# Performance work log

Measured on AMD Instinct MI355X. Metric: run time of the kernel, lower is better.

## Reference

```python
import jax, jax.numpy as jnp
import numpy as np

# ---- geometry constants (LinearProbeGeom) ----
N_DET, N_T = 128, 2048
NX, NY = 128, 256
PITCH, DT = 3.0e-4, 2.5e-8
C_SOUND = 1540.0
X0, DX = 0.0, 3.0e-4
Y0, DY = 1.0e-3, 1.5e-4
ARRAY_X0, ARRAY_Y = 0.0, 0.0

_freq = np.fft.rfftfreq(N_T, d=DT).astype(np.float32)
OMEGA = jnp.asarray(2.0 * np.pi * _freq, dtype=jnp.float32)            # [n_f]
KX = jnp.asarray((2.0 * np.pi * np.fft.fftfreq(N_DET, d=PITCH)).astype(np.float32))  # [n_det]
_fw = np.ones(_freq.shape[0], dtype=np.float32)
if _fw.shape[0] > 2:
    _fw[1:-1] = 2.0
if N_T % 2 == 0 and _fw.shape[0] > 1:
    _fw[-1] = 1.0
FREQ_W = jnp.asarray(_fw)                                              # [n_f]
XC = jnp.asarray((X0 + np.arange(NX) * DX - ARRAY_X0).astype(np.float32))  # [nx]
YC = jnp.asarray((Y0 + np.arange(NY) * DY - ARRAY_Y).astype(np.float32))   # [ny]


def setup_inputs() -> dict:
    key = jax.random.key(0)
    sino = jax.random.normal(key, (8, 2, N_DET, N_T), dtype=jnp.float32)
    # Hann window apodization (non-trainable buffer in the torch module)
    win = 0.5 - 0.5 * np.cos(2 * np.pi * np.arange(N_DET) / max(N_DET - 1, 1))
    apod = jnp.asarray(win.astype(np.float32))
    return {"sino": sino, "apod": apod}


def reference(sino, apod):
    B, C, n_det, n_t = sino.shape
    eps = jnp.finfo(jnp.float32).eps
    # per-(B,C) standardization over (n_det, n_t)
    mean = sino.mean(axis=(-2, -1), keepdims=True)
    sn = sino - mean
    std = jnp.sqrt(jnp.mean(sn * sn, axis=(-2, -1), keepdims=True) + eps)
    sn = sn / std
    sw = sn * apod[None, None, :, None]
    # temporal rFFT then spatial FFT over detectors -> [B,C,n_det,n_f] complex64
    spec = jnp.fft.fft(jnp.fft.rfft(sw, axis=-1), axis=2)
    kz_sq = (OMEGA / C_SOUND)[None, :] ** 2 - (KX ** 2)[:, None]       # [n_det,n_f]
    kz = jnp.sqrt(jnp.clip(kz_sq, 0.0))
    spec = spec * (kz_sq > 0).astype(spec.dtype)
    # phase factors (vectorized over all ny depths -> one big contraction)
    phase_x = jnp.exp(1j * KX[:, None] * XC[None, :]).astype(spec.dtype)        # [n_det,nx]
    phase_y = jnp.exp(1j * YC[:, None, None] * kz[None, :, :]).astype(spec.dtype)  # [ny,n_det,n_f]
    specw = spec * FREQ_W.astype(spec.dtype)[None, None, None, :]
    band = jnp.einsum('bcdf,ydf->bcyd', specw, phase_y)                # sum over freq
    img_c = jnp.einsum('bcyd,dx->bcyx', band, phase_x)                 # [B,C,ny,nx]
    img = jnp.abs(img_c).astype(sino.dtype)
    norm = jnp.maximum(apod.sum(), eps) * jnp.maximum(FREQ_W.sum(), eps)
    return img / norm
```

## Files before the change

### kernel.cpp

```cpp
#include <hip/hip_runtime.h>
#include <math.h>

#define N_DETC 128
#define N_TC   2048
#define N_FC   1025
#define N_FP   1056
#define NXC    128
#define NYC    256
#define NBCC   16

#define MPAD(i) ((i) + ((i) >> 5))

typedef short bf16x8 __attribute__((ext_vector_type(8)));
typedef float f32x4  __attribute__((ext_vector_type(4)));

__device__ __forceinline__ float2 cmulf(float2 a, float2 b){
    return make_float2(a.x*b.x - a.y*b.y, a.x*b.y + a.y*b.x);
}

#if __has_builtin(__builtin_amdgcn_sinf) && __has_builtin(__builtin_amdgcn_cosf)
__device__ __forceinline__ float sin_rev(float tf){ return __builtin_amdgcn_sinf(tf); }
__device__ __forceinline__ float cos_rev(float tf){ return __builtin_amdgcn_cosf(tf); }
#else
__device__ __forceinline__ float sin_rev(float tf){ return __sinf(6.28318530718f * tf); }
__device__ __forceinline__ float cos_rev(float tf){ return __cosf(6.28318530718f * tf); }
#endif

__device__ __forceinline__ ushort cvt_bf16(float x){
    uint u = __float_as_uint(x);
    return (ushort)((u + 0x7FFFu + ((u >> 16) & 1u)) >> 16);
}

__global__ __launch_bounds__(256) void k_stats1(const float* __restrict__ sino,
                                                float* __restrict__ psum,
                                                float* __restrict__ psq){
    int bc    = blockIdx.x >> 6;
    int chunk = blockIdx.x & 63;
    const float4* p = (const float4*)(sino + (size_t)bc * (N_DETC * N_TC)) + (size_t)chunk * 1024;
    float s = 0.f, q = 0.f;
    #pragma unroll
    for (int i = 0; i < 4; ++i){
        float4 v = p[threadIdx.x + i * 256];
        s += v.x + v.y + v.z + v.w;
        q += v.x*v.x + v.y*v.y + v.z*v.z + v.w*v.w;
    }
    #pragma unroll
    for (int m = 1; m < 64; m <<= 1){
        s += __shfl_xor(s, m, 64);
        q += __shfl_xor(q, m, 64);
    }
    __shared__ float ls[4], lq[4];
    int w = threadIdx.x >> 6, lane = threadIdx.x & 63;
    if (lane == 0){ ls[w] = s; lq[w] = q; }
    __syncthreads();
    if (threadIdx.x == 0){
        psum[blockIdx.x] = ls[0] + ls[1] + ls[2] + ls[3];
        psq[blockIdx.x]  = lq[0] + lq[1] + lq[2] + lq[3];
    }
}

__global__ __launch_bounds__(256) void k_tfft(const float* __restrict__ sino,
                                              const float* __restrict__ apod,
                                              const float* __restrict__ psum,
                                              const float* __restrict__ psq,
                                              float2* __restrict__ spec){
    int row = blockIdx.x;
    int bc = row >> 7, d = row & 127;
    __shared__ float2 z[1055];
    __shared__ float sm[2];
    int tid = threadIdx.x;
    if (tid < 64){
        float s = psum[bc * 64 + tid], q = psq[bc * 64 + tid];
        #pragma unroll
        for (int m = 1; m < 64; m <<= 1){
            s += __shfl_xor(s, m, 64);
            q += __shfl_xor(q, m, 64);
        }
        if (tid == 0){
            const float inv_n = 1.f / (float)(N_DETC * N_TC);
            float mean = s * inv_n;
            float var  = q * inv_n - mean * mean;
            sm[0] = mean;
            sm[1] = rsqrtf(fmaxf(var, 0.f) + 1.1920929e-7f);
        }
    }
    __syncthreads();
    float mean = sm[0];
    float scl  = sm[1] * apod[d];
    const float2* p = (const float2*)(sino + (size_t)row * N_TC);
    for (int n = tid; n < 1024; n += 256){
        float2 v = p[n];
        int r = __brev((unsigned)n) >> 22;
        z[MPAD(r)] = make_float2((v.x - mean) * scl, (v.y - mean) * scl);
    }
    __syncthreads();
    #pragma unroll
    for (int st = 0; st < 5; ++st){
        int h = 1 << (2 * st);
        int q = tid;
        int k = q & (h - 1);
        int g = q >> (2 * st);
        int base = (g << (2 * st + 2)) + k;
        float2 x0 = z[MPAD(base)];
        float2 x1 = z[MPAD(base + h)];
        float2 x2 = z[MPAD(base + 2 * h)];
        float2 x3 = z[MPAD(base + 3 * h)];
        float a1 = -(float)M_PI * (float)k / (float)h;
        float s1, c1; __sincosf(a1, &s1, &c1);
        float a2 = 0.5f * a1;
        float s2, c2; __sincosf(a2, &s2, &c2);
        float2 t1 = make_float2(x1.x * c1 - x1.y * s1, x1.x * s1 + x1.y * c1);
        float2 t3 = make_float2(x3.x * c1 - x3.y * s1, x3.x * s1 + x3.y * c1);
        float2 y0 = make_float2(x0.x + t1.x, x0.y + t1.y);
        float2 y1 = make_float2(x0.x - t1.x, x0.y - t1.y);
        float2 y2 = make_float2(x2.x + t3.x, x2.y + t3.y);
        float2 y3 = make_float2(x2.x - t3.x, x2.y - t3.y);
        float2 u = make_float2(y2.x * c2 - y2.y * s2, y2.x * s2 + y2.y * c2);
        float2 v = make_float2(y3.x * c2 - y3.y * s2, y3.x * s2 + y3.y * c2);
        float2 w = make_float2(v.y, -v.x);
        z[MPAD(base)]         = make_float2(y0.x + u.x, y0.y + u.y);
        z[MPAD(base + 2 * h)] = make_float2(y0.x - u.x, y0.y - u.y);
        z[MPAD(base + h)]     = make_float2(y1.x + w.x, y1.y + w.y);
        z[MPAD(base + 3 * h)] = make_float2(y1.x - w.x, y1.y - w.y);
        __syncthreads();
    }
    float2* o = spec + (size_t)row * N_FC;
    for (int k = tid; k < 1025; k += 256){
        float2 A  = z[MPAD(k & 1023)];
        float2 Bv = z[MPAD((1024 - k) & 1023)];
        float Br = Bv.x, Bi = -Bv.y;
        float Er = 0.5f * (A.x + Br), Ei = 0.5f * (A.y + Bi);
        float Dr = 0.5f * (A.x - Br), Di = 0.5f * (A.y - Bi);
        float Or = Di, Oi = -Dr;
        float ang = -(float)M_PI * (float)k * (1.0f / 1024.0f);
        float sn, cs; __sincosf(ang, &sn, &cs);
        float Xr = Er + cs * Or - sn * Oi;
        float Xi = Ei + cs * Oi + sn * Or;
        o[k] = make_float2(Xr, Xi);
    }
}

__global__ __launch_bounds__(256) void k_dft(const float2* __restrict__ spec,
                                             ushort* __restrict__ Arp,
                                             ushort* __restrict__ Aip,
                                             float4* __restrict__ kzJ){
    int bid = blockIdx.x;
    int ft = bid >> 4, bc = bid & 15;
    int f0 = ft << 5;
    int tid = threadIdx.x;
    __shared__ float2 tile[128][33];
    __shared__ ushort stAr[128][40];
    __shared__ ushort stAi[128][40];

    int fl  = tid & 31;
    int kd0 = tid >> 5;
    int f = f0 + fl;
    bool fok = (f <= 1024);
    float fr = (float)f * 19531.25f;
    float oc = fr * (1.0f / 1540.0f);

    #pragma unroll
    for (int i = 0; i < 16; ++i){
        int kd = kd0 + (i << 3);
        int rkd = __brev((unsigned)kd) >> 25;
        float2 v = fok ? spec[((size_t)(bc * 128 + kd)) * N_FC + f] : make_float2(0.f, 0.f);
        tile[rkd][fl] = v;
    }
    if (bc == 0){
        #pragma unroll
        for (int i = 0; i < 16; ++i){
            int kd = kd0 + (i << 3);
            int sdx = (kd < 64) ? kd : kd - 128;
            float bb = (float)sdx * 26.0416666f;
            float kq = oc * oc - bb * bb;
            float kzr = (fok && kq > 0.f) ? sqrtf(kq) : 0.f;
            float tj = 1.5e-4f * kzr;
            tj -= floorf(tj);
            kzJ[(size_t)kd * N_FP + f] = make_float4(kzr, cos_rev(tj), sin_rev(tj), 0.f);
        }
    }
    __syncthreads();
    #pragma unroll
    for (int st = 0; st < 3; ++st){
        int h = 1 << (2 * st);
        #pragma unroll
        for (int it = 0; it < 4; ++it){
            int task = tid + (it << 8);
            int ff = task & 31;
            int q  = task >> 5;
            int k = q & (h - 1);
            int g = q >> (2 * st);
            int base = (g << (2 * st + 2)) + k;
            float2 x0 = tile[base][ff];
            float2 x1 = tile[base + h][ff];
            float2 x2 = tile[base + 2 * h][ff];
            float2 x3 = tile[base + 3 * h][ff];
            float a1 = -(float)M_PI * (float)k / (float)h;
            float s1, c1; __sincosf(a1, &s1, &c1);
            float a2 = 0.5f * a1;
            float s2, c2; __sincosf(a2, &s2, &c2);
            float2 t1 = make_float2(x1.x * c1 - x1.y * s1, x1.x * s1 + x1.y * c1);
            float2 t3 = make_float2(x3.x * c1 - x3.y * s1, x3.x * s1 + x3.y * c1);
            float2 y0 = make_float2(x0.x + t1.x, x0.y + t1.y);
            float2 y1 = make_float2(x0.x - t1.x, x0.y - t1.y);
            float2 y2 = make_float2(x2.x + t3.x, x2.y + t3.y);
            float2 y3 = make_float2(x2.x - t3.x, x2.y - t3.y);
            float2 u = make_float2(y2.x * c2 - y2.y * s2, y2.x * s2 + y2.y * c2);
            float2 v = make_float2(y3.x * c2 - y3.y * s2, y3.x * s2 + y3.y * c2);
            float2 w = make_float2(v.y, -v.x);
            tile[base][ff]         = make_float2(y0.x + u.x, y0.y + u.y);
            tile[base + 2 * h][ff] = make_float2(y0.x - u.x, y0.y - u.y);
            tile[base + h][ff]     = make_float2(y1.x + w.x, y1.y + w.y);
            tile[base + 3 * h][ff] = make_float2(y1.x - w.x, y1.y - w.y);
        }
        __syncthreads();
    }
    #pragma unroll
    for (int it = 0; it < 8; ++it){
        int task = tid + (it << 8);
        int ff = task & 31, j = task >> 5;
        int i1 = j, i2 = j + 64;
        float ang = -(float)M_PI * (float)j * (1.0f / 64.0f);
        float sn, cs; __sincosf(ang, &sn, &cs);
        float2 u = tile[i1][ff], v = tile[i2][ff];
        float2 t = make_float2(v.x * cs - v.y * sn, v.x * sn + v.y * cs);
        tile[i1][ff] = make_float2(u.x + t.x, u.y + t.y);
        tile[i2][ff] = make_float2(u.x - t.x, u.y - t.y);
    }
    __syncthreads();
    float fw = (f == 0 || f == 1024) ? 1.f : 2.f;
    #pragma unroll
    for (int i = 0; i < 16; ++i){
        int kd = kd0 + (i << 3);
        int sdx = (kd < 64) ? kd : kd - 128;
        float bb = (float)sdx * 26.0416666f;
        float m = (fok && (oc * oc - bb * bb > 0.f)) ? fw : 0.f;
        float2 v = tile[kd][fl];
        stAr[kd][fl] = cvt_bf16(v.x * m);
        stAi[kd][fl] = cvt_bf16(v.y * m);
    }
    __syncthreads();
    int kds = tid >> 1, hf = tid & 1;
    size_t rowoff = ((size_t)kds * 16 + bc) * N_FP + f0 + hf * 16;
    uint4 r0 = *(const uint4*)&stAr[kds][hf * 16];
    uint4 r1 = *(const uint4*)&stAr[kds][hf * 16 + 8];
    uint4 i0 = *(const uint4*)&stAi[kds][hf * 16];
    uint4 i1v = *(const uint4*)&stAi[kds][hf * 16 + 8];
    ((uint4*)(Arp + rowoff))[0] = r0;
    ((uint4*)(Arp + rowoff))[1] = r1;
    ((uint4*)(Aip + rowoff))[0] = i0;
    ((uint4*)(Aip + rowoff))[1] = i1v;
}

__global__ __launch_bounds__(512) void k_band(const ushort* __restrict__ Ar,
                                              const ushort* __restrict__ Ai,
                                              const float4* __restrict__ kzJ,
                                              float2* __restrict__ band_p){
    int blk = blockIdx.x;
    int fc = blk & 1;
    int yh = (blk >> 1) & 1;
    int kd = blk >> 2;
    int nt = fc ? 17 : 16;
    int tid  = threadIdx.x;
    int wid  = tid >> 6;
    int lane = tid & 63;
    int fp = tid & 15;
    int yq = tid >> 4;
    float ymg = 1.0e-3f + 1.5e-4f * (float)(yh * 128 + yq * 4);

    __shared__ ushort Bls[2][2][128][40];

    int arow = lane & 15;
    int koff = (lane >> 4) * 8;
    int ylocal = wid * 16 + arow;
    const ushort* Arp = Ar + ((size_t)kd * 16 + arow) * N_FP + koff + fc * 512;
    const ushort* Aip = Ai + ((size_t)kd * 16 + arow) * N_FP + koff + fc * 512;
    const float4* kjb = kzJ + (size_t)kd * N_FP + fc * 512;

    auto GENC = [&](float4 k0, float4 k1, int buf){
        float t0 = ymg * k0.x; t0 -= floorf(t0);
        float t1 = ymg * k1.x; t1 -= floorf(t1);
        float cA = cos_rev(t0), sA = sin_rev(t0);
        float cB = cos_rev(t1), sB = sin_rev(t1);
        #pragma unroll
        for (int j = 0; j < 4; ++j){
            int y = yq * 4 + j;
            uint br, bi;
            asm("v_cvt_pk_bf16_f32 %0, %1, %2" : "=v"(br) : "v"(cA), "v"(cB));
            asm("v_cvt_pk_bf16_f32 %0, %1, %2" : "=v"(bi) : "v"(sA), "v"(sB));
            *(uint*)&Bls[buf][0][y][fp * 2] = br;
            *(uint*)&Bls[buf][1][y][fp * 2] = bi;
            if (j < 3){
                float nA = fmaf(cA, k0.y, -(sA * k0.z));
                float mA = fmaf(sA, k0.y,  (cA * k0.z));
                cA = nA; sA = mA;
                float nB = fmaf(cB, k1.y, -(sB * k1.z));
                float mB = fmaf(sB, k1.y,  (cB * k1.z));
                cB = nB; sB = mB;
            }
        }
    };

    f32x4 P1 = {0.f,0.f,0.f,0.f}, P2 = P1, P3 = P1, P4 = P1;

    bf16x8 car = *(const bf16x8*)(Arp);
    bf16x8 cai = *(const bf16x8*)(Aip);
    GENC(kjb[fp * 2], kjb[fp * 2 + 1], 0);
    __syncthreads();

    for (int t = 0; t < nt; ++t){
        bf16x8 nar, nai;
        float4 k0, k1;
        if (t < nt - 1){
            nar = *(const bf16x8*)(Arp + (t + 1) * 32);
            nai = *(const bf16x8*)(Aip + (t + 1) * 32);
            k0 = kjb[(t + 1) * 32 + fp * 2];
            k1 = kjb[(t + 1) * 32 + fp * 2 + 1];
        }
        int buf = t & 1;
        bf16x8 br = *(const bf16x8*)&Bls[buf][0][ylocal][koff];
        bf16x8 bi = *(const bf16x8*)&Bls[buf][1][ylocal][koff];
        P1 = __builtin_amdgcn_mfma_f32_16x16x32_bf16(car, br, P1, 0, 0, 0);
        P2 = __builtin_amdgcn_mfma_f32_16x16x32_bf16(cai, bi, P2, 0, 0, 0);
        P3 = __builtin_amdgcn_mfma_f32_16x16x32_bf16(car, bi, P3, 0, 0, 0);
        P4 = __builtin_amdgcn_mfma_f32_16x16x32_bf16(cai, br, P4, 0, 0, 0);
        if (t < nt - 1){
            GENC(k0, k1, buf ^ 1);
        }
        __syncthreads();
        if (t < nt - 1){ car = nar; cai = nai; }
    }

    int y = yh * 128 + wid * 16 + (lane & 15);
    #pragma unroll
    for (int r = 0; r < 4; ++r){
        int bc = (lane >> 4) * 4 + r;
        band_p[(((size_t)fc * 128 + kd) * 16 + bc) * 256 + y] = make_float2(P1[r] - P2[r], P3[r] + P4[r]);
    }
}

__global__ __launch_bounds__(256) void k_final(const float2* __restrict__ band_p,
                                               const float* __restrict__ apod,
                                               float* __restrict__ out){
    int blk = blockIdx.x;
    int bc = blk >> 5, yt = blk & 31;
    __shared__ float2 tile[128][9];
    __shared__ float asum;
    int tid = threadIdx.x;
    if (tid < 64){
        float a = apod[tid] + apod[tid + 64];
        #pragma unroll
        for (int m = 1; m < 64; m <<= 1) a += __shfl_xor(a, m, 64);
        if (tid == 0) asum = a;
    }
    #pragma unroll
    for (int k2 = 0; k2 < 4; ++k2){
        int idx = tid + k2 * 256;
        int kd = idx >> 3, yi = idx & 7;
        size_t o0 = (((size_t)0 * 128 + kd) * 16 + bc) * 256 + yt * 8 + yi;
        size_t o1 = (((size_t)1 * 128 + kd) * 16 + bc) * 256 + yt * 8 + yi;
        float2 a = band_p[o0], b = band_p[o1];
        int rkd = __brev((unsigned)kd) >> 25;
        tile[rkd][yi] = make_float2(a.x + b.x, a.y + b.y);
    }
    __syncthreads();
    #pragma unroll
    for (int st = 0; st < 3; ++st){
        int h = 1 << (2 * st);
        int q  = tid >> 3;
        int yi = tid & 7;
        int k = q & (h - 1);
        int g = q >> (2 * st);
        int base = (g << (2 * st + 2)) + k;
        float2 x0 = tile[base][yi];
        float2 x1 = tile[base + h][yi];
        float2 x2 = tile[base + 2 * h][yi];
        float2 x3 = tile[base + 3 * h][yi];
        float a1 = (float)M_PI * (float)k / (float)h;
        float s1, c1; __sincosf(a1, &s1, &c1);
        float a2 = 0.5f * a1;
        float s2, c2; __sincosf(a2, &s2, &c2);
        float2 t1 = make_float2(x1.x * c1 - x1.y * s1, x1.x * s1 + x1.y * c1);
        float2 t3 = make_float2(x3.x * c1 - x3.y * s1, x3.x * s1 + x3.y * c1);
        float2 y0 = make_float2(x0.x + t1.x, x0.y + t1.y);
        float2 y1 = make_float2(x0.x - t1.x, x0.y - t1.y);
        float2 y2 = make_float2(x2.x + t3.x, x2.y + t3.y);
        float2 y3 = make_float2(x2.x - t3.x, x2.y - t3.y);
        float2 u = make_float2(y2.x * c2 - y2.y * s2, y2.x * s2 + y2.y * c2);
        float2 v = make_float2(y3.x * c2 - y3.y * s2, y3.x * s2 + y3.y * c2);
        float2 w = make_float2(-v.y, v.x);
        tile[base][yi]         = make_float2(y0.x + u.x, y0.y + u.y);
        tile[base + 2 * h][yi] = make_float2(y0.x - u.x, y0.y - u.y);
        tile[base + h][yi]     = make_float2(y1.x + w.x, y1.y + w.y);
        tile[base + 3 * h][yi] = make_float2(y1.x - w.x, y1.y - w.y);
        __syncthreads();
    }
    #pragma unroll
    for (int it = 0; it < 2; ++it){
        int task = tid + (it << 8);
        int yi = task & 7, j = task >> 3;
        float ang = (float)M_PI * (float)j * (1.0f / 64.0f);
        float sn, cs; __sincosf(ang, &sn, &cs);
        float2 u = tile[j][yi], v = tile[j + 64][yi];
        float2 t = make_float2(v.x * cs - v.y * sn, v.x * sn + v.y * cs);
        tile[j][yi]      = make_float2(u.x + t.x, u.y + t.y);
        tile[j + 64][yi] = make_float2(u.x - t.x, u.y - t.y);
    }
    __syncthreads();
    float invnorm = 1.f / (fmaxf(asum, 1.1920929e-7f) * 2048.f);
    #pragma unroll
    for (int k2 = 0; k2 < 4; ++k2){
        int idx = tid + k2 * 256;
        int x = idx & 127, yi = idx >> 7;
        float2 v = tile[x][yi];
        int y = yt * 8 + yi;
        out[((size_t)bc * 256 + y) * 128 + x] = sqrtf(v.x * v.x + v.y * v.y) * invnorm;
    }
}

extern "C" void kernel_launch(void* const* d_in, const int* in_sizes, int n_in,
                              void* d_out, int out_size, void* d_ws, size_t ws_size,
                              hipStream_t stream){
    const float* sino = (const float*)d_in[0];
    const float* apod = (const float*)d_in[1];
    float* out = (float*)d_out;
    float* W = (float*)d_ws;
    float* psum = W + 64;
    float* psq  = W + 1088;
    float2* spec  = (float2*)(W + 2112);
    ushort* Arp   = (ushort*)(W + 2112 + 4198400);
    ushort* Aip   = Arp + (size_t)16 * 128 * N_FP;
    float4* kzJ   = (float4*)(W + 2112 + 4198400 + 2162688);
    float2* band_p = spec;

    k_stats1<<<NBCC * 64, 256, 0, stream>>>(sino, psum, psq);
    k_tfft  <<<NBCC * N_DETC, 256, 0, stream>>>(sino, apod, psum, psq, spec);
    k_dft   <<<33 * 16, 256, 0, stream>>>(spec, Arp, Aip, kzJ);
    k_band  <<<512, 512, 0, stream>>>(Arp, Aip, kzJ, band_p);
    k_final <<<NBCC * 32, 256, 0, stream>>>(band_p, apod, out);
}
```

Before: 69.83 us.

## Fuse stats into temporal FFT, defer normalization, store spectrum as bf16

Removes the separate statistics kernel. Each temporal-FFT block now accumulates per-row sum and sum-of-squares while running the FFT on raw data. Mean subtraction (only the DC bin changes) and the apodization/std scaling move into the spatial DFT kernel, which works because the FFT is linear. The intermediate spectrum is packed to bf16 pairs, halving its write and read traffic, at the cost of reduced precision before normalization.

```diff
diff --git a/kernel.cpp b/kernel.cpp
--- a/kernel.cpp
+++ b/kernel.cpp
@@ -31,75 +31,41 @@
     return (ushort)((u + 0x7FFFu + ((u >> 16) & 1u)) >> 16);
 }
 
-__global__ __launch_bounds__(256) void k_stats1(const float* __restrict__ sino,
-                                                float* __restrict__ psum,
-                                                float* __restrict__ psq){
-    int bc    = blockIdx.x >> 6;
-    int chunk = blockIdx.x & 63;
-    const float4* p = (const float4*)(sino + (size_t)bc * (N_DETC * N_TC)) + (size_t)chunk * 1024;
+__global__ __launch_bounds__(256) void k_tfft(const float* __restrict__ sino,
+                                              float* __restrict__ psum,
+                                              float* __restrict__ psq,
+                                              uint* __restrict__ spec_u){
+    int row = blockIdx.x;
+    __shared__ float2 z[1055];
+    __shared__ float ls[4], lq[4];
+    int tid = threadIdx.x;
+    const float2* p = (const float2*)(sino + (size_t)row * N_TC);
     float s = 0.f, q = 0.f;
-    #pragma unroll
-    for (int i = 0; i < 4; ++i){
-        float4 v = p[threadIdx.x + i * 256];
-        s += v.x + v.y + v.z + v.w;
-        q += v.x*v.x + v.y*v.y + v.z*v.z + v.w*v.w;
+    for (int n = tid; n < 1024; n += 256){
+        float2 v = p[n];
+        s += v.x + v.y;
+        q += v.x * v.x + v.y * v.y;
+        int r = __brev((unsigned)n) >> 22;
+        z[MPAD(r)] = v;
     }
     #pragma unroll
     for (int m = 1; m < 64; m <<= 1){
         s += __shfl_xor(s, m, 64);
         q += __shfl_xor(q, m, 64);
     }
-    __shared__ float ls[4], lq[4];
-    int w = threadIdx.x >> 6, lane = threadIdx.x & 63;
+    int w = tid >> 6, lane = tid & 63;
     if (lane == 0){ ls[w] = s; lq[w] = q; }
     __syncthreads();
-    if (threadIdx.x == 0){
-        psum[blockIdx.x] = ls[0] + ls[1] + ls[2] + ls[3];
-        psq[blockIdx.x]  = lq[0] + lq[1] + lq[2] + lq[3];
-    }
-}
-
-__global__ __launch_bounds__(256) void k_tfft(const float* __restrict__ sino,
-                                              const float* __restrict__ apod,
-                                              const float* __restrict__ psum,
-                                              const float* __restrict__ psq,
-                                              float2* __restrict__ spec){
-    int row = blockIdx.x;
-    int bc = row >> 7, d = row & 127;
-    __shared__ float2 z[1055];
-    __shared__ float sm[2];
-    int tid = threadIdx.x;
-    if (tid < 64){
-        float s = psum[bc * 64 + tid], q = psq[bc * 64 + tid];
-        #pragma unroll
-        for (int m = 1; m < 64; m <<= 1){
-            s += __shfl_xor(s, m, 64);
-            q += __shfl_xor(q, m, 64);
-        }
-        if (tid == 0){
-            const float inv_n = 1.f / (float)(N_DETC * N_TC);
-            float mean = s * inv_n;
-            float var  = q * inv_n - mean * mean;
-            sm[0] = mean;
-            sm[1] = rsqrtf(fmaxf(var, 0.f) + 1.1920929e-7f);
-        }
-    }
-    __syncthreads();
-    float mean = sm[0];
-    float scl  = sm[1] * apod[d];
-    const float2* p = (const float2*)(sino + (size_t)row * N_TC);
-    for (int n = tid; n < 1024; n += 256){
-        float2 v = p[n];
-        int r = __brev((unsigned)n) >> 22;
-        z[MPAD(r)] = make_float2((v.x - mean) * scl, (v.y - mean) * scl);
-    }
-    __syncthreads();
+    if (tid == 0){
+        psum[row] = ls[0] + ls[1] + ls[2] + ls[3];
+        psq[row]  = lq[0] + lq[1] + lq[2] + lq[3];
+    }
     #pragma unroll
     for (int st = 0; st < 5; ++st){
         int h = 1 << (2 * st);
-        int q = tid;
-        int k = q & (h - 1);
-        int g = q >> (2 * st);
+        int qd = tid;
+        int k = qd & (h - 1);
+        int g = qd >> (2 * st);
         int base = (g << (2 * st + 2)) + k;
         float2 x0 = z[MPAD(base)];
         float2 x1 = z[MPAD(base + h)];
@@ -117,14 +83,14 @@
         float2 y3 = make_float2(x2.x - t3.x, x2.y - t3.y);
         float2 u = make_float2(y2.x * c2 - y2.y * s2, y2.x * s2 + y2.y * c2);
         float2 v = make_float2(y3.x * c2 - y3.y * s2, y3.x * s2 + y3.y * c2);
-        float2 w = make_float2(v.y, -v.x);
+        float2 wv = make_float2(v.y, -v.x);
         z[MPAD(base)]         = make_float2(y0.x + u.x, y0.y + u.y);
         z[MPAD(base + 2 * h)] = make_float2(y0.x - u.x, y0.y - u.y);
-        z[MPAD(base + h)]     = make_float2(y1.x + w.x, y1.y + w.y);
-        z[MPAD(base + 3 * h)] = make_float2(y1.x - w.x, y1.y - w.y);
+        z[MPAD(base + h)]     = make_float2(y1.x + wv.x, y1.y + wv.y);
+        z[MPAD(base + 3 * h)] = make_float2(y1.x - wv.x, y1.y - wv.y);
         __syncthreads();
     }
-    float2* o = spec + (size_t)row * N_FC;
+    uint* o = spec_u + (size_t)row * N_FC;
     for (int k = tid; k < 1025; k += 256){
         float2 A  = z[MPAD(k & 1023)];
         float2 Bv = z[MPAD((1024 - k) & 1023)];
@@ -136,11 +102,16 @@
         float sn, cs; __sincosf(ang, &sn, &cs);
         float Xr = Er + cs * Or - sn * Oi;
         float Xi = Ei + cs * Oi + sn * Or;
-        o[k] = make_float2(Xr, Xi);
-    }
-}
-
-__global__ __launch_bounds__(256) void k_dft(const float2* __restrict__ spec,
+        uint pk;
+        asm("v_cvt_pk_bf16_f32 %0, %1, %2" : "=v"(pk) : "v"(Xr), "v"(Xi));
+        o[k] = pk;
+    }
+}
+
+__global__ __launch_bounds__(256) void k_dft(const uint* __restrict__ spec_u,
+                                             const float* __restrict__ psum,
+                                             const float* __restrict__ psq,
+                                             const float* __restrict__ apod,
                                              ushort* __restrict__ Arp,
                                              ushort* __restrict__ Aip,
                                              float4* __restrict__ kzJ){
@@ -151,6 +122,26 @@
     __shared__ float2 tile[128][33];
     __shared__ ushort stAr[128][40];
     __shared__ ushort stAi[128][40];
+    __shared__ float sm[2];
+
+    if (tid < 64){
+        float s = psum[bc * 128 + tid] + psum[bc * 128 + 64 + tid];
+        float q = psq[bc * 128 + tid] + psq[bc * 128 + 64 + tid];
+        #pragma unroll
+        for (int m = 1; m < 64; m <<= 1){
+            s += __shfl_xor(s, m, 64);
+            q += __shfl_xor(q, m, 64);
+        }
+        if (tid == 0){
+            const float inv_n = 1.f / (float)(N_DETC * N_TC);
+            float mean = s * inv_n;
+            float var  = q * inv_n - mean * mean;
+            sm[0] = mean;
+            sm[1] = rsqrtf(fmaxf(var, 0.f) + 1.1920929e-7f);
+        }
+    }
+    __syncthreads();
+    float mean = sm[0], invstd = sm[1];
 
     int fl  = tid & 31;
     int kd0 = tid >> 5;
@@ -163,8 +154,12 @@
     for (int i = 0; i < 16; ++i){
         int kd = kd0 + (i << 3);
         int rkd = __brev((unsigned)kd) >> 25;
-        float2 v = fok ? spec[((size_t)(bc * 128 + kd)) * N_FC + f] : make_float2(0.f, 0.f);
-        tile[rkd][fl] = v;
+        uint u = fok ? spec_u[((size_t)(bc * 128 + kd)) * N_FC + f] : 0u;
+        float vr = __uint_as_float(u << 16);
+        float vi = __uint_as_float(u & 0xFFFF0000u);
+        if (f == 0) vr -= mean * 2048.f;
+        float sc = apod[kd] * invstd;
+        tile[rkd][fl] = make_float2(vr * sc, vi * sc);
     }
     if (bc == 0){
         #pragma unroll
@@ -425,17 +420,16 @@
     const float* apod = (const float*)d_in[1];
     float* out = (float*)d_out;
     float* W = (float*)d_ws;
-    float* psum = W + 64;
-    float* psq  = W + 1088;
-    float2* spec  = (float2*)(W + 2112);
-    ushort* Arp   = (ushort*)(W + 2112 + 4198400);
-    ushort* Aip   = Arp + (size_t)16 * 128 * N_FP;
-    float4* kzJ   = (float4*)(W + 2112 + 4198400 + 2162688);
-    float2* band_p = spec;
-
-    k_stats1<<<NBCC * 64, 256, 0, stream>>>(sino, psum, psq);
-    k_tfft  <<<NBCC * N_DETC, 256, 0, stream>>>(sino, apod, psum, psq, spec);
-    k_dft   <<<33 * 16, 256, 0, stream>>>(spec, Arp, Aip, kzJ);
+    float* psum = W;
+    float* psq  = W + 2048;
+    uint*   spec_u = (uint*)(W + 4096);
+    ushort* Arp    = (ushort*)(W + 4096 + 2099200);
+    ushort* Aip    = Arp + (size_t)16 * 128 * N_FP;
+    float4* kzJ    = (float4*)(W + 4096 + 2099200 + 2162688);
+    float2* band_p = (float2*)(W + 4096 + 2099200 + 2162688 + 540672);
+
+    k_tfft  <<<NBCC * N_DETC, 256, 0, stream>>>(sino, psum, psq, spec_u);
+    k_dft   <<<33 * 16, 256, 0, stream>>>(spec_u, psum, psq, apod, Arp, Aip, kzJ);
     k_band  <<<512, 512, 0, stream>>>(Arp, Aip, kzJ, band_p);
     k_final <<<NBCC * 32, 256, 0, stream>>>(band_p, apod, out);
 }
```

After: 65.47 us. -6.2%, faster.
